# Kernel optimization log

Hardware: AMD Instinct MI355X
Metric: run time of the kernel (lower is better)

The kernel has to match this reference:

```python
import jax, jax.numpy as jnp
import numpy as np

N = 100000      # nodes
E = 1600000     # directed edges (avg degree 16)
F_IN = 128
HID = 64
OUT = 10


def setup_inputs() -> dict:
    key = jax.random.key(0)
    ks = jax.random.split(key, 6)
    x = jax.random.normal(ks[0], (N, F_IN), dtype=jnp.float32)
    edge_index = jax.random.randint(ks[1], (2, E), 0, N, dtype=jnp.int32)
    # Glorot-scaled weights like PyG's GCNConv.lin; bias added post-aggregation
    W1 = jax.random.normal(ks[2], (F_IN, HID), dtype=jnp.float32) * np.float32(1.0 / np.sqrt(F_IN))
    b1 = jnp.zeros((HID,), dtype=jnp.float32)
    W2 = jax.random.normal(ks[3], (HID, OUT), dtype=jnp.float32) * np.float32(1.0 / np.sqrt(HID))
    b2 = jnp.zeros((OUT,), dtype=jnp.float32)
    return {"x": x, "edge_index": edge_index, "W1": W1, "b1": b1, "W2": W2, "b2": b2}


def _gcn_norm(edge_index, num_nodes):
    """Add self-loops and compute symmetric normalization D^-1/2 A D^-1/2 (PyG gcn_norm)."""
    loops = jnp.arange(num_nodes, dtype=edge_index.dtype)
    src = jnp.concatenate([edge_index[0], loops])
    dst = jnp.concatenate([edge_index[1], loops])
    deg = jax.ops.segment_sum(jnp.ones_like(dst, dtype=jnp.float32), dst, num_segments=num_nodes)
    dinv = jnp.where(deg > 0, jax.lax.rsqrt(deg), 0.0)  # inf -> 0 as in PyG
    norm = dinv[src] * dinv[dst]  # [E+N]
    return src, dst, norm


def _gcn_conv(x, src, dst, norm, W, b, num_nodes):
    h = x @ W                                   # transform first (smaller dim aggregated)
    msg = h[src] * norm[:, None]                # gather + scale
    agg = jax.ops.segment_sum(msg, dst, num_segments=num_nodes)  # scatter-add
    return agg + b


def reference(x, edge_index, W1, b1, W2, b2):
    src, dst, norm = _gcn_norm(edge_index, N)
    h = jax.nn.relu(_gcn_conv(x, src, dst, norm, W1, b1, N))
    # F.dropout(training=self.training): identity in eval mode
    out = _gcn_conv(h, src, dst, norm, W2, b2, N)
    return out
```

## Files before the change

kernel.cpp:

```cpp
#include <hip/hip_runtime.h>
#include <hip/hip_fp16.h>

static constexpr int F = 128;
static constexpr int H = 64;
static constexpr int O = 10;
static constexpr int PSU = 6;
static constexpr int NBUK_MAX = 256;
static constexpr int CAP = 12288;
static constexpr int ESCAP = 14336;
static constexpr int EPB = 4096;
static constexpr int XPAD = 136;

typedef _Float16 half8 __attribute__((ext_vector_type(8)));
typedef float floatx4 __attribute__((ext_vector_type(4)));

__global__ __launch_bounds__(256) void k_init(int* __restrict__ bcntg,
                                              const float* __restrict__ W1,
                                              __half* __restrict__ W1f,
                                              unsigned* __restrict__ yN,
                                              unsigned* __restrict__ zsN) {
    int b = blockIdx.x, t = threadIdx.x;
    if (b == 0) {
        bcntg[t] = 0;
        if (t < 32) yN[t] = 0u;
        if (t < PSU) zsN[t] = 0u;
    } else {
        int i = (b - 1) * 256 + t;
        int j = i & 7, lane = (i >> 3) & 63, sc = i >> 9;
        int s = sc >> 2, c = sc & 3;
        int k = s * 32 + (lane >> 4) * 8 + j;
        int nn = c * 16 + (lane & 15);
        W1f[i] = __float2half(W1[k * H + nn]);
    }
}

__global__ __launch_bounds__(256) void k_bin(const int* __restrict__ src,
                                             const int* __restrict__ dst,
                                             int* __restrict__ bcntg,
                                             unsigned* __restrict__ ebuf, int e_total) {
    __shared__ int hist[NBUK_MAX];
    __shared__ int base[NBUK_MAX];
    __shared__ int loc[NBUK_MAX];
    int t = threadIdx.x;
    hist[t] = 0;
    loc[t] = 0;
    __syncthreads();
    int i0 = blockIdx.x * EPB;
    int i1 = min(i0 + EPB, e_total);
    int i = i0 + 4 * t;
    for (; i + 3 < i1; i += 1024) {
        int4 d4 = *(const int4*)&dst[i];
        atomicAdd(&hist[d4.x >> 9], 1);
        atomicAdd(&hist[d4.y >> 9], 1);
        atomicAdd(&hist[d4.z >> 9], 1);
        atomicAdd(&hist[d4.w >> 9], 1);
    }
    for (; i < i1; ++i) atomicAdd(&hist[dst[i] >> 9], 1);
    __syncthreads();
    if (hist[t] > 0) base[t] = atomicAdd(&bcntg[t], hist[t]);
    __syncthreads();
    i = i0 + 4 * t;
    for (; i + 3 < i1; i += 1024) {
        int4 s4 = *(const int4*)&src[i];
        int4 d4 = *(const int4*)&dst[i];
#pragma unroll
        for (int u = 0; u < 4; ++u) {
            int s = (&s4.x)[u], d = (&d4.x)[u];
            int b = d >> 9;
            int r = base[b] + atomicAdd(&loc[b], 1);
            if (r < CAP)
                ebuf[(size_t)b * CAP + r] = ((unsigned)(d & 511) << 17) | (unsigned)s;
        }
    }
    for (; i < i1; ++i) {
        int s = src[i], d = dst[i];
        int b = d >> 9;
        int r = base[b] + atomicAdd(&loc[b], 1);
        if (r < CAP)
            ebuf[(size_t)b * CAP + r] = ((unsigned)(d & 511) << 17) | (unsigned)s;
    }
}

__global__ __launch_bounds__(256) void k_bsort(
    const unsigned* __restrict__ ebuf, const int* __restrict__ bcntg,
    int* __restrict__ rowbeg, int* __restrict__ degp, float* __restrict__ dinv,
    int* __restrict__ esrc, int n_nodes) {
    __shared__ int hc[512];
    __shared__ int sa[512];
    __shared__ int sb[512];
    int t = threadIdx.x, b = blockIdx.x, n0 = b << 9;
    hc[t] = 0;
    hc[t + 256] = 0;
    __syncthreads();
    int cb = min(bcntg[b], CAP);
    const unsigned* eb = ebuf + (size_t)b * CAP;
    int i = 4 * t;
    for (; i + 3 < cb; i += 1024) {
        uint4 e4 = *(const uint4*)&eb[i];
        atomicAdd(&hc[e4.x >> 17], 1);
        atomicAdd(&hc[e4.y >> 17], 1);
        atomicAdd(&hc[e4.z >> 17], 1);
        atomicAdd(&hc[e4.w >> 17], 1);
    }
    for (; i < cb; ++i) atomicAdd(&hc[eb[i] >> 17], 1);
    __syncthreads();
#pragma unroll
    for (int u = 0; u < 2; ++u) {
        int ii = t + 256 * u;
        sa[ii] = (hc[ii] + 15) & ~15;
    }
    __syncthreads();
    int* A = sa;
    int* Bp = sb;
    for (int off = 1; off < 512; off <<= 1) {
#pragma unroll
        for (int u = 0; u < 2; ++u) {
            int ii = t + 256 * u;
            int v = A[ii];
            if (ii >= off) v += A[ii - off];
            Bp[ii] = v;
        }
        __syncthreads();
        int* tmp = A; A = Bp; Bp = tmp;
    }
#pragma unroll
    for (int u = 0; u < 2; ++u) {
        int ii = t + 256 * u;
        int cnt = hc[ii];
        int cp = (cnt + 15) & ~15;
        int excl = A[ii] - cp;
        Bp[ii] = excl;
        int n = n0 + ii;
        if (n < n_nodes) {
            rowbeg[n] = b * ESCAP + excl;
            degp[n] = cp;
            dinv[n] = rsqrtf((float)cnt + 1.0f);
        }
    }
    __syncthreads();
    int* es = esrc + (size_t)b * ESCAP;
    i = 4 * t;
    for (; i + 3 < cb; i += 1024) {
        uint4 e4 = *(const uint4*)&eb[i];
#pragma unroll
        for (int u = 0; u < 4; ++u) {
            unsigned e = (&e4.x)[u];
            int r = atomicAdd(&Bp[e >> 17], 1);
            es[r] = (int)(e & 0x1FFFFu);
        }
    }
    for (; i < cb; ++i) {
        unsigned e = eb[i];
        int r = atomicAdd(&Bp[e >> 17], 1);
        es[r] = (int)(e & 0x1FFFFu);
    }
    __syncthreads();
#pragma unroll
    for (int u = 0; u < 2; ++u) {
        int ii = t + 256 * u;
        int end = A[ii];
        for (int p = Bp[ii]; p < end; ++p) es[p] = n_nodes;
    }
}

__global__ __launch_bounds__(256, 4) void k_gemm1(
    const float* __restrict__ x, const __half* __restrict__ W1f,
    const float* __restrict__ dinv, __half* __restrict__ y, int n_nodes) {
    __shared__ __half xh[64 * XPAD];
    const int tid = threadIdx.x;
    const int lane = tid & 63;
    const int w = tid >> 6;
    const int row0 = blockIdx.x * 64;

    half8 bf[16];
    const uint4* wf = (const uint4*)W1f;
#pragma unroll
    for (int sc = 0; sc < 16; ++sc) {
        union { uint4 u; half8 h; } tmp;
        tmp.u = wf[sc * 64 + lane];
        bf[sc] = tmp.h;
    }

    for (int i = tid; i < 64 * 32; i += 256) {
        int r = i >> 5, k4 = i & 31;
        int gr = row0 + r;
        if (gr < n_nodes) {
            float4 v = *(const float4*)&x[(size_t)gr * F + 4 * k4];
            __half2 p0 = __floats2half2_rn(v.x, v.y);
            __half2 p1 = __floats2half2_rn(v.z, v.w);
            uint2 pk = make_uint2(*(unsigned*)&p0, *(unsigned*)&p1);
            *(uint2*)&xh[r * XPAD + 4 * k4] = pk;
        }
    }
    __syncthreads();

    const int m16 = lane & 15, quad = lane >> 4;
    floatx4 acc[4];
#pragma unroll
    for (int c = 0; c < 4; ++c) acc[c] = (floatx4){0.f, 0.f, 0.f, 0.f};
#pragma unroll
    for (int s = 0; s < 4; ++s) {
        union { uint4 u; half8 h; } ua;
        ua.u = *(const uint4*)&xh[(16 * w + m16) * XPAD + s * 32 + quad * 8];
#pragma unroll
        for (int c = 0; c < 4; ++c)
            acc[c] = __builtin_amdgcn_mfma_f32_16x16x32_f16(ua.h, bf[s * 4 + c],
                                                            acc[c], 0, 0, 0);
    }
#pragma unroll
    for (int r = 0; r < 4; ++r) {
        int grow = row0 + 16 * w + quad * 4 + r;
        if (grow < n_nodes) {
            float d = dinv[grow];
#pragma unroll
            for (int c = 0; c < 4; ++c)
                y[(size_t)grow * H + c * 16 + m16] = __float2half(acc[c][r] * d);
        }
    }
}

__global__ __launch_bounds__(256) void k_gather1(
    const uint2* __restrict__ yq, const int* __restrict__ rowbeg,
    const int* __restrict__ degp, const int* __restrict__ esrc,
    const float* __restrict__ dinv, const float* __restrict__ b1,
    uint2* __restrict__ hq, int n_nodes) {
    const int l = threadIdx.x & 63;
    const int g = l >> 4;
    const int c = l & 15;
    const int n = blockIdx.x * 4 + (threadIdx.x >> 6);
    if (n >= n_nodes) return;
    const int beg = rowbeg[n];
    const int dp = degp[n];
    const int idx = esrc[beg + l];
    float2 aA = make_float2(0.f, 0.f);
    float2 aB = make_float2(0.f, 0.f);
    if (g == 0) {
        uint2 v = yq[(size_t)n * 16 + c];
        float2 fA = __half22float2(*(const __half2*)&v.x);
        float2 fB = __half22float2(*(const __half2*)&v.y);
        aA.x += fA.x; aA.y += fA.y; aB.x += fB.x; aB.y += fB.y;
    }
    const int dlim = min(dp, 64);
    for (int k = 0; k < dlim; k += 16) {
#pragma unroll
        for (int u = 0; u < 4; ++u) {
            int s = __shfl(idx, k + 4 * u + g, 64);
            uint2 v = yq[(size_t)s * 16 + c];
            float2 fA = __half22float2(*(const __half2*)&v.x);
            float2 fB = __half22float2(*(const __half2*)&v.y);
            aA.x += fA.x; aA.y += fA.y; aB.x += fB.x; aB.y += fB.y;
        }
    }
    for (int kk = 64; kk < dp; kk += 4) {
        int s = esrc[beg + kk + g];
        uint2 v = yq[(size_t)s * 16 + c];
        float2 fA = __half22float2(*(const __half2*)&v.x);
        float2 fB = __half22float2(*(const __half2*)&v.y);
        aA.x += fA.x; aA.y += fA.y; aB.x += fB.x; aB.y += fB.y;
    }
#pragma unroll
    for (int off = 16; off <= 32; off <<= 1) {
        aA.x += __shfl_xor(aA.x, off, 64);
        aA.y += __shfl_xor(aA.y, off, 64);
        aB.x += __shfl_xor(aB.x, off, 64);
        aB.y += __shfl_xor(aB.y, off, 64);
    }
    if (g == 0) {
        float4 bb = ((const float4*)b1)[c];
        float d = dinv[n];
        float h0 = fmaxf(fmaf(d, aA.x, bb.x), 0.0f);
        float h1 = fmaxf(fmaf(d, aA.y, bb.y), 0.0f);
        float h2 = fmaxf(fmaf(d, aB.x, bb.z), 0.0f);
        float h3 = fmaxf(fmaf(d, aB.y, bb.w), 0.0f);
        __half2 p0 = __floats2half2_rn(h0, h1);
        __half2 p1 = __floats2half2_rn(h2, h3);
        hq[(size_t)n * 16 + c] = make_uint2(*(const unsigned*)&p0, *(const unsigned*)&p1);
    }
}

__global__ __launch_bounds__(256) void k_zs(
    const __half* __restrict__ h, const float* __restrict__ W2,
    const float* __restrict__ dinv, unsigned* __restrict__ zs_u, int n_nodes) {
    __shared__ unsigned zbuf[256 * PSU];
    const int t = threadIdx.x;
    const int n0 = blockIdx.x * 256;
    const int n = n0 + t;
    if (n < n_nodes) {
        float acc[O];
#pragma unroll
        for (int j = 0; j < O; ++j) acc[j] = 0.f;
        const __half2* hr = (const __half2*)(h + (size_t)n * H);
#pragma unroll
        for (int k2 = 0; k2 < H / 2; ++k2) {
            float2 hv = __half22float2(hr[k2]);
#pragma unroll
            for (int j = 0; j < O; ++j) {
                acc[j] = fmaf(hv.x, W2[(2 * k2 + 0) * O + j], acc[j]);
                acc[j] = fmaf(hv.y, W2[(2 * k2 + 1) * O + j], acc[j]);
            }
        }
        float d = dinv[n];
#pragma unroll
        for (int q = 0; q < O / 2; ++q) {
            __half2 p = __floats2half2_rn(acc[2 * q] * d, acc[2 * q + 1] * d);
            zbuf[t * PSU + q] = *(const unsigned*)&p;
        }
        zbuf[t * PSU + 5] = 0u;
    }
    __syncthreads();
    int total = (min(n0 + 256, n_nodes) - n0) * PSU;
    unsigned* zo = zs_u + (size_t)n0 * PSU;
    for (int i = t; i < total; i += 256) zo[i] = zbuf[i];
}

__global__ __launch_bounds__(256) void k_gather2(
    const unsigned* __restrict__ zs_u, const int* __restrict__ rowbeg,
    const int* __restrict__ degp, const int* __restrict__ esrc,
    const float* __restrict__ dinv, const float* __restrict__ b2,
    float* __restrict__ out, int n_nodes) {
    const int l = threadIdx.x & 63;
    const int j = l & 7;
    const int sbase = l & ~7;
    const int jj = (j < 5) ? j : 5;
    const int n = blockIdx.x * 32 + (threadIdx.x >> 3);
    if (n >= n_nodes) return;
    const int beg = rowbeg[n];
    const int dp = degp[n];
    unsigned v0 = zs_u[(size_t)n * PSU + jj];
    float2 acc = __half22float2(*(const __half2*)&v0);
    for (int k0 = 0; k0 < dp; k0 += 8) {
        int idx = esrc[beg + k0 + j];
#pragma unroll
        for (int e = 0; e < 8; ++e) {
            int s = __shfl(idx, sbase + e, 64);
            unsigned v = zs_u[(size_t)s * PSU + jj];
            float2 f = __half22float2(*(const __half2*)&v);
            acc.x += f.x;
            acc.y += f.y;
        }
    }
    if (j < 5) {
        float2 bb = ((const float2*)b2)[j];
        float d = dinv[n];
        float2 o = make_float2(fmaf(d, acc.x, bb.x), fmaf(d, acc.y, bb.y));
        *(float2*)&out[(size_t)n * O + 2 * j] = o;
    }
}

static inline size_t align256(size_t v) { return (v + 255) & ~(size_t)255; }

extern "C" void kernel_launch(void* const* d_in, const int* in_sizes, int n_in,
                              void* d_out, int out_size, void* d_ws, size_t ws_size,
                              hipStream_t stream) {
    const float* x  = (const float*)d_in[0];
    const int*   ei = (const int*)d_in[1];
    const float* W1 = (const float*)d_in[2];
    const float* b1 = (const float*)d_in[3];
    const float* W2 = (const float*)d_in[4];
    const float* b2 = (const float*)d_in[5];
    float* out = (float*)d_out;

    const int N = in_sizes[0] / F;
    const int E = in_sizes[1] / 2;
    const int* src = ei;
    const int* dst = ei + E;
    const int NBUK = (N + 511) >> 9;

    char* base = (char*)d_ws;
    __half* y = (__half*)base;
    size_t ysz = align256((size_t)(N + 1) * H * 2);
    char* hreg = base + ysz;
    __half* h = (__half*)hreg;
    unsigned* ebuf = (unsigned*)hreg;
    __half* W1f = (__half*)(hreg + (size_t)N * H * 2 - (size_t)F * H * 2);
    size_t hsz = align256((size_t)N * H * 2);
    char* zreg = hreg + hsz;
    unsigned* zs_u = (unsigned*)zreg;
    size_t zsz = align256((size_t)(N + 1) * PSU * 4);
    float* dinv = (float*)(zreg + zsz);
    int* rowbeg = (int*)(dinv + N);
    int* degp = rowbeg + N;
    int* bcntg = degp + N;
    int* esrc = bcntg + 256;

    const int nb_bin = (E + EPB - 1) / EPB;

    k_init<<<1 + F * H / 256, 256, 0, stream>>>(bcntg, W1, W1f,
                                                (unsigned*)(y + (size_t)N * H),
                                                zs_u + (size_t)N * PSU);
    k_bin<<<nb_bin, 256, 0, stream>>>(src, dst, bcntg, ebuf, E);
    k_bsort<<<NBUK, 256, 0, stream>>>(ebuf, bcntg, rowbeg, degp, dinv, esrc, N);
    k_gemm1<<<(N + 63) / 64, 256, 0, stream>>>(x, W1f, dinv, y, N);
    k_gather1<<<(N + 3) / 4, 256, 0, stream>>>((const uint2*)y, rowbeg, degp,
                                               esrc, dinv, b1, (uint2*)h, N);
    k_zs<<<(N + 255) / 256, 256, 0, stream>>>(h, W2, dinv, zs_u, N);
    k_gather2<<<(N + 31) / 32, 256, 0, stream>>>(zs_u, rowbeg, degp, esrc,
                                                 dinv, b2, out, N);
}
```

Baseline: 200.5 us.

## Fuse layer-2 linear transform into layer-1 gather kernel

Merges k_gather1 and k_zs: after aggregating and applying bias+ReLU, each wavefront multiplies its 64-wide hidden row by W2 (staged in shared memory) and reduces across lanes with shuffles, then writes the scaled fp16 z row directly. This removes the intermediate h buffer write/read (N*64 fp16) and one kernel launch. It adds per-block W2 loads into LDS, a __syncthreads before the early-return, and extra shuffle work in the gather kernel.

```diff
diff --git a/kernel.cpp b/kernel.cpp
--- a/kernel.cpp
+++ b/kernel.cpp
@@ -219,11 +219,14 @@
     }
 }
 
-__global__ __launch_bounds__(256) void k_gather1(
+__global__ __launch_bounds__(256) void k_gather1z(
     const uint2* __restrict__ yq, const int* __restrict__ rowbeg,
     const int* __restrict__ degp, const int* __restrict__ esrc,
     const float* __restrict__ dinv, const float* __restrict__ b1,
-    uint2* __restrict__ hq, int n_nodes) {
+    const float* __restrict__ W2, unsigned* __restrict__ zs_u, int n_nodes) {
+    __shared__ float w2s[H * O];
+    for (int i = threadIdx.x; i < H * O; i += 256) w2s[i] = W2[i];
+    __syncthreads();
     const int l = threadIdx.x & 63;
     const int g = l >> 4;
     const int c = l & 15;
@@ -265,52 +268,39 @@
         aB.x += __shfl_xor(aB.x, off, 64);
         aB.y += __shfl_xor(aB.y, off, 64);
     }
-    if (g == 0) {
-        float4 bb = ((const float4*)b1)[c];
-        float d = dinv[n];
-        float h0 = fmaxf(fmaf(d, aA.x, bb.x), 0.0f);
-        float h1 = fmaxf(fmaf(d, aA.y, bb.y), 0.0f);
-        float h2 = fmaxf(fmaf(d, aB.x, bb.z), 0.0f);
-        float h3 = fmaxf(fmaf(d, aB.y, bb.w), 0.0f);
-        __half2 p0 = __floats2half2_rn(h0, h1);
-        __half2 p1 = __floats2half2_rn(h2, h3);
-        hq[(size_t)n * 16 + c] = make_uint2(*(const unsigned*)&p0, *(const unsigned*)&p1);
-    }
-}
-
-__global__ __launch_bounds__(256) void k_zs(
-    const __half* __restrict__ h, const float* __restrict__ W2,
-    const float* __restrict__ dinv, unsigned* __restrict__ zs_u, int n_nodes) {
-    __shared__ unsigned zbuf[256 * PSU];
-    const int t = threadIdx.x;
-    const int n0 = blockIdx.x * 256;
-    const int n = n0 + t;
-    if (n < n_nodes) {
-        float acc[O];
-#pragma unroll
-        for (int j = 0; j < O; ++j) acc[j] = 0.f;
-        const __half2* hr = (const __half2*)(h + (size_t)n * H);
-#pragma unroll
-        for (int k2 = 0; k2 < H / 2; ++k2) {
-            float2 hv = __half22float2(hr[k2]);
-#pragma unroll
-            for (int j = 0; j < O; ++j) {
-                acc[j] = fmaf(hv.x, W2[(2 * k2 + 0) * O + j], acc[j]);
-                acc[j] = fmaf(hv.y, W2[(2 * k2 + 1) * O + j], acc[j]);
-            }
-        }
-        float d = dinv[n];
-#pragma unroll
-        for (int q = 0; q < O / 2; ++q) {
-            __half2 p = __floats2half2_rn(acc[2 * q] * d, acc[2 * q + 1] * d);
-            zbuf[t * PSU + q] = *(const unsigned*)&p;
-        }
-        zbuf[t * PSU + 5] = 0u;
-    }
-    __syncthreads();
-    int total = (min(n0 + 256, n_nodes) - n0) * PSU;
-    unsigned* zo = zs_u + (size_t)n0 * PSU;
-    for (int i = t; i < total; i += 256) zo[i] = zbuf[i];
+    const float4 bb = ((const float4*)b1)[c];
+    const float d = dinv[n];
+    const float h0 = fmaxf(fmaf(d, aA.x, bb.x), 0.0f);
+    const float h1 = fmaxf(fmaf(d, aA.y, bb.y), 0.0f);
+    const float h2 = fmaxf(fmaf(d, aB.x, bb.z), 0.0f);
+    const float h3 = fmaxf(fmaf(d, aB.y, bb.w), 0.0f);
+    const float* wr = &w2s[(4 * c) * O];
+    const int ja = 2 * g;
+    float sa0 = h0 * wr[0 * O + ja]     + h1 * wr[1 * O + ja]
+              + h2 * wr[2 * O + ja]     + h3 * wr[3 * O + ja];
+    float sa1 = h0 * wr[0 * O + ja + 1] + h1 * wr[1 * O + ja + 1]
+              + h2 * wr[2 * O + ja + 1] + h3 * wr[3 * O + ja + 1];
+    float sb0 = h0 * wr[0 * O + 8]      + h1 * wr[1 * O + 8]
+              + h2 * wr[2 * O + 8]      + h3 * wr[3 * O + 8];
+    float sb1 = h0 * wr[0 * O + 9]      + h1 * wr[1 * O + 9]
+              + h2 * wr[2 * O + 9]      + h3 * wr[3 * O + 9];
+#pragma unroll
+    for (int m = 1; m <= 8; m <<= 1) {
+        sa0 += __shfl_xor(sa0, m, 64);
+        sa1 += __shfl_xor(sa1, m, 64);
+        sb0 += __shfl_xor(sb0, m, 64);
+        sb1 += __shfl_xor(sb1, m, 64);
+    }
+    const size_t rb = (size_t)n * PSU;
+    if (c == 0) {
+        __half2 pa = __floats2half2_rn(sa0 * d, sa1 * d);
+        zs_u[rb + g] = *(const unsigned*)&pa;
+    }
+    if (l == 1) {
+        __half2 pb = __floats2half2_rn(sb0 * d, sb1 * d);
+        zs_u[rb + 4] = *(const unsigned*)&pb;
+    }
+    if (l == 2) zs_u[rb + 5] = 0u;
 }
 
 __global__ __launch_bounds__(256) void k_gather2(
@@ -370,7 +360,6 @@
     __half* y = (__half*)base;
     size_t ysz = align256((size_t)(N + 1) * H * 2);
     char* hreg = base + ysz;
-    __half* h = (__half*)hreg;
     unsigned* ebuf = (unsigned*)hreg;
     __half* W1f = (__half*)(hreg + (size_t)N * H * 2 - (size_t)F * H * 2);
     size_t hsz = align256((size_t)N * H * 2);
@@ -391,9 +380,8 @@
     k_bin<<<nb_bin, 256, 0, stream>>>(src, dst, bcntg, ebuf, E);
     k_bsort<<<NBUK, 256, 0, stream>>>(ebuf, bcntg, rowbeg, degp, dinv, esrc, N);
     k_gemm1<<<(N + 63) / 64, 256, 0, stream>>>(x, W1f, dinv, y, N);
-    k_gather1<<<(N + 3) / 4, 256, 0, stream>>>((const uint2*)y, rowbeg, degp,
-                                               esrc, dinv, b1, (uint2*)h, N);
-    k_zs<<<(N + 255) / 256, 256, 0, stream>>>(h, W2, dinv, zs_u, N);
+    k_gather1z<<<(N + 3) / 4, 256, 0, stream>>>((const uint2*)y, rowbeg, degp,
+                                                esrc, dinv, b1, W2, zs_u, N);
     k_gather2<<<(N + 31) / 32, 256, 0, stream>>>(zs_u, rowbeg, degp, esrc,
                                                  dinv, b2, out, N);
 }
```

New measurement: 218.8 us. 9.2% more time.
